# Performance work log

Measured on AMD Instinct MI355X. Metric: run time of the kernel, lower is better.

Reference implementation:

```python
import jax, jax.numpy as jnp
import numpy as np

B, N, D, H, DK = 4, 2048, 1024, 16, 64  # batch, seq, model_dim, heads, key_dim (= value_dim)
NEG = -1e9


def setup_inputs() -> dict:
    key = jax.random.key(0)
    ks = jax.random.split(key, 5)
    X = jax.random.normal(ks[0], (B, N, D), dtype=jnp.float32)
    # causal additive mask [N, N]; module slices mask[:N, :M] and adds to logits
    mask = jnp.where(jnp.tril(jnp.ones((N, N), dtype=bool)), 0.0, NEG).astype(jnp.float32)
    s = 1.0 / np.sqrt(D)
    Wq = jax.random.normal(ks[1], (D, H * DK), dtype=jnp.float32) * s
    Wk = jax.random.normal(ks[2], (D, H * DK), dtype=jnp.float32) * s
    Wv = jax.random.normal(ks[3], (D, H * DK), dtype=jnp.float32) * s
    Wo = jax.random.normal(ks[4], (H * DK, D), dtype=jnp.float32) * s
    return {"X": X, "mask": mask, "Wq": Wq, "Wk": Wk, "Wv": Wv, "Wo": Wo}


def reference(X, mask, Wq, Wk, Wv, Wo):
    # Linear projections (bias=False), then split heads: [B,N,H,DK] -> [B,H,N,DK]
    Q = (X @ Wq).reshape(B, N, H, DK).transpose(0, 2, 1, 3)
    K = (X @ Wk).reshape(B, N, H, DK).transpose(0, 2, 1, 3)
    V = (X @ Wv).reshape(B, N, H, DK).transpose(0, 2, 1, 3)
    # full [B,H,N,N] attention logits (module materializes it explicitly)
    att = jnp.einsum('bhnd,bhmd->bhnm', Q, K) / jnp.sqrt(jnp.float32(DK))
    # dropout is in eval mode here -> identity; then additive mask[:N,:M]
    att = att + mask[:N, :N]
    prob = jax.nn.softmax(att, axis=-1)
    values = jnp.einsum('bhnm,bhmd->bhnd', prob, V)
    values_cat = values.transpose(0, 2, 1, 3).reshape(B, N, H * DK)
    return values_cat @ Wo
```

## Files before the change

kernel.cpp:

```cpp
#include <hip/hip_runtime.h>

typedef __fp16   f2  __attribute__((ext_vector_type(2)));
typedef _Float16 h4  __attribute__((ext_vector_type(4)));
typedef _Float16 v8h __attribute__((ext_vector_type(8)));
typedef float    v4f __attribute__((ext_vector_type(4)));
struct f2x2 { f2 lo, hi; };

constexpr int Bn = 4, Nn = 2048, Dn = 1024, Hn = 16, DKn = 64, Mn = 8192;

__device__ __forceinline__ void load_lds16(const _Float16* g, _Float16* l) {
    __builtin_amdgcn_global_load_lds(
        (const __attribute__((address_space(1))) void*)g,
        (__attribute__((address_space(3))) void*)l, 16, 0, 0);
}

__global__ __launch_bounds__(256) void cast_f16(const float* __restrict__ x,
                                                _Float16* __restrict__ y) {
    const int i = blockIdx.x * 256 + threadIdx.x;
    const float4 v = ((const float4*)x)[i];
    h4 o; o[0] = (_Float16)v.x; o[1] = (_Float16)v.y;
    o[2] = (_Float16)v.z; o[3] = (_Float16)v.w;
    ((h4*)y)[i] = o;
}

__global__ __launch_bounds__(256) void castW4(const float* __restrict__ Wq,
                                              const float* __restrict__ Wk,
                                              const float* __restrict__ Wv,
                                              const float* __restrict__ Wo,
                                              _Float16* __restrict__ Wqkv,
                                              _Float16* __restrict__ Wto) {
    __shared__ float tile[32][33];
    const int which = blockIdx.x >> 10, bid = blockIdx.x & 1023;
    const float* W = which == 0 ? Wq : which == 1 ? Wk : which == 2 ? Wv : Wo;
    _Float16* Dst = which < 3 ? (Wqkv + ((size_t)which << 20)) : Wto;
    const int bx = bid & 31, by = bid >> 5;
    const int t = threadIdx.x;
    const int r = t >> 3, c4 = (t & 7) * 4;
    const float4 v = *(const float4*)&W[(size_t)(by * 32 + r) * Dn + bx * 32 + c4];
    tile[r][c4 + 0] = v.x; tile[r][c4 + 1] = v.y;
    tile[r][c4 + 2] = v.z; tile[r][c4 + 3] = v.w;
    __syncthreads();
    h4 o;
    o[0] = (_Float16)tile[c4 + 0][r];
    o[1] = (_Float16)tile[c4 + 1][r];
    o[2] = (_Float16)tile[c4 + 2][r];
    o[3] = (_Float16)tile[c4 + 3][r];
    *(h4*)&Dst[(size_t)(bx * 32 + r) * Dn + by * 32 + c4] = o;
}

#define GEMM_KLOOP(Abase, Bbase)                                                    \
    v4f acc[4][4];                                                                  \
    _Pragma("unroll") for (int i = 0; i < 4; ++i)                                   \
        _Pragma("unroll") for (int j = 0; j < 4; ++j) acc[i][j] = v4f{0,0,0,0};     \
    const int sw8 = (quad ^ (l16 >> 2)) * 8;                                        \
    for (int k0 = 0; k0 < Dn; k0 += 32) {                                           \
        __syncthreads();                                                            \
        _Pragma("unroll") for (int jj = 0; jj < 2; ++jj) {                          \
            const int ci = jj * 256 + w * 64 + lane;                                \
            const int rs = ci >> 2, cs = ci & 3;                                    \
            const int gc = (cs ^ ((rs >> 2) & 3)) * 8;                              \
            load_lds16(Abase + (size_t)rs * Dn + k0 + gc, &As[(jj*256 + w*64) * 8]);\
            load_lds16(Bbase + (size_t)rs * Dn + k0 + gc, &Bs[(jj*256 + w*64) * 8]);\
        }                                                                           \
        __syncthreads();                                                            \
        v8h a[4], b[4];                                                             \
        _Pragma("unroll") for (int i = 0; i < 4; ++i)                               \
            a[i] = *(const v8h*)&As[(wm*64 + i*16 + l16) * 32 + sw8];               \
        _Pragma("unroll") for (int j = 0; j < 4; ++j)                               \
            b[j] = *(const v8h*)&Bs[(wn*64 + j*16 + l16) * 32 + sw8];               \
        _Pragma("unroll") for (int i = 0; i < 4; ++i)                               \
            _Pragma("unroll") for (int j = 0; j < 4; ++j)                           \
                acc[i][j] = __builtin_amdgcn_mfma_f32_16x16x32_f16(a[i], b[j],      \
                                                                   acc[i][j],0,0,0);\
    }

__global__ __launch_bounds__(256) void gemmqkv(const _Float16* __restrict__ A,
                                               const _Float16* __restrict__ Wt,
                                               _Float16* __restrict__ Qo,
                                               _Float16* __restrict__ Ko,
                                               _Float16* __restrict__ Vo)
{
    __shared__ __align__(16) _Float16 As[128 * 32];
    __shared__ __align__(16) _Float16 Bs[128 * 32];
    const int t = threadIdx.x, lane = t & 63, w = t >> 6;
    const int quad = lane >> 4, l16 = lane & 15;
    const int wm = w >> 1, wn = w & 1;
    const int bx = blockIdx.x % 24, by = blockIdx.x / 24;
    const int m0 = by * 128, n0 = bx * 128;
    const _Float16* Abase = A + (size_t)m0 * Dn;
    const _Float16* Bbase = Wt + (size_t)n0 * Dn;

    GEMM_KLOOP(Abase, Bbase)

    const int sec = n0 >> 10;
    if (sec < 2) {
        _Float16* C = sec ? Ko : Qo;
        const float scale = sec ? 1.0f : 0.125f * 1.44269504f;
#pragma unroll
        for (int i = 0; i < 4; ++i) {
            const int mbase = m0 + wm * 64 + i * 16 + quad * 4;
#pragma unroll
            for (int j = 0; j < 4; ++j) {
                const int nl = (n0 + wn * 64 + j * 16 + l16) & 1023;
                const int h = nl >> 6, dk = nl & 63;
#pragma unroll
                for (int r = 0; r < 4; ++r) {
                    const int m = mbase + r, b = m >> 11, nr = m & (Nn - 1);
                    C[((size_t)(b * Hn + h) * Nn + nr) * DKn + dk] = (_Float16)(acc[i][j][r] * scale);
                }
            }
        }
    } else {
#pragma unroll
        for (int i = 0; i < 4; ++i) {
            const int mbase = m0 + wm * 64 + i * 16 + quad * 4;
            const int b = mbase >> 11, nr = mbase & (Nn - 1);
#pragma unroll
            for (int j = 0; j < 4; ++j) {
                const int nl = (n0 + wn * 64 + j * 16 + l16) & 1023;
                const int h = nl >> 6, dk = nl & 63;
                h4 o; o[0] = (_Float16)acc[i][j][0]; o[1] = (_Float16)acc[i][j][1];
                o[2] = (_Float16)acc[i][j][2]; o[3] = (_Float16)acc[i][j][3];
                *(h4*)&Vo[((size_t)(b * Hn + h) * DKn + dk) * Nn + nr] = o;
            }
        }
    }
}

__global__ __launch_bounds__(256) void gemmo(const _Float16* __restrict__ A,
                                             const _Float16* __restrict__ Wt,
                                             float* __restrict__ C)
{
    __shared__ __align__(16) _Float16 As[128 * 32];
    __shared__ __align__(16) _Float16 Bs[128 * 32];
    const int t = threadIdx.x, lane = t & 63, w = t >> 6;
    const int quad = lane >> 4, l16 = lane & 15;
    const int wm = w >> 1, wn = w & 1;
    const int bx = blockIdx.x & 7, by = blockIdx.x >> 3;
    const int m0 = by * 128, n0 = bx * 128;
    const _Float16* Abase = A + (size_t)m0 * Dn;
    const _Float16* Bbase = Wt + (size_t)n0 * Dn;

    GEMM_KLOOP(Abase, Bbase)

#pragma unroll
    for (int i = 0; i < 4; ++i) {
        const int mbase = m0 + wm * 64 + i * 16 + quad * 4;
#pragma unroll
        for (int j = 0; j < 4; ++j) {
            const int n = n0 + wn * 64 + j * 16 + l16;
#pragma unroll
            for (int r = 0; r < 4; ++r)
                C[(size_t)(mbase + r) * Dn + n] = acc[i][j][r];
        }
    }
}

__global__ __launch_bounds__(256) void flashv5(const _Float16* __restrict__ Q,
                                               const _Float16* __restrict__ K,
                                               const _Float16* __restrict__ Vt,
                                               _Float16* __restrict__ O)
{
    __shared__ __align__(16) _Float16 KS[64 * 64];
    __shared__ __align__(16) _Float16 VS[64 * 64];
    __shared__ __align__(16) _Float16 Ps[4][32 * 64];

    const int t = threadIdx.x;
    const int lane = t & 63, w = t >> 6;
    const int quad = lane >> 4, l16 = lane & 15;
    const int bh = blockIdx.x & 63;
    const int qtile = 15 - (blockIdx.x >> 6);
    const int b = bh >> 4, h = bh & 15;
    const int qb = qtile * 128 + w * 32;

    const _Float16* Qg = Q  + (size_t)bh * Nn * DKn;
    const _Float16* Kg = K  + (size_t)bh * Nn * DKn;
    const _Float16* Vg = Vt + (size_t)bh * DKn * Nn;

    auto stage = [&](int kt) {
        const int k0 = kt * 64;
#pragma unroll
        for (int jj = 0; jj < 2; ++jj) {
            const int ci = jj * 256 + w * 64 + lane;
            const int r = ci >> 3, c = ci & 7;
            const int gc = (c ^ (r & 7)) * 8;
            load_lds16(Kg + (size_t)(k0 + r) * DKn + gc, &KS[(jj * 256 + w * 64) * 8]);
            load_lds16(Vg + (size_t)r * Nn + k0 + gc,    &VS[(jj * 256 + w * 64) * 8]);
        }
    };
#define SWZ(arr, r, c) (*(const v8h*)&(arr)[(r) * 64 + (((c) ^ ((r) & 7)) * 8)])

    v8h qf[2][2];
#pragma unroll
    for (int qq = 0; qq < 2; ++qq)
#pragma unroll
        for (int ks = 0; ks < 2; ++ks)
            qf[qq][ks] = *(const v8h*)&Qg[(size_t)(qb + qq * 16 + l16) * DKn + ks * 32 + quad * 8];

    v8h ones;
#pragma unroll
    for (int i = 0; i < 8; ++i) ones[i] = (_Float16)1.0f;

    v4f o[2][4];
#pragma unroll
    for (int mq = 0; mq < 2; ++mq)
#pragma unroll
        for (int nt = 0; nt < 4; ++nt) o[mq][nt] = v4f{0.f, 0.f, 0.f, 0.f};
    v4f ol[2] = {v4f{0.f, 0.f, 0.f, 0.f}, v4f{0.f, 0.f, 0.f, 0.f}};

    const int NKT  = 2 * qtile + 2;
    const int diag = 2 * qtile + (w >> 1);

    for (int kt = 0; kt < NKT; ++kt) {
        stage(kt);
        __syncthreads();
        if (kt <= diag) {
            const int k0 = kt * 64;
            auto ptile = [&](bool domask) {
#pragma unroll
                for (int kk = 0; kk < 4; ++kk) {
                    v4f s0 = v4f{0.f, 0.f, 0.f, 0.f}, s1 = v4f{0.f, 0.f, 0.f, 0.f};
#pragma unroll
                    for (int ks = 0; ks < 2; ++ks) {
                        const v8h ak = SWZ(KS, kk * 16 + l16, ks * 4 + quad);
                        s0 = __builtin_amdgcn_mfma_f32_16x16x32_f16(ak, qf[0][ks], s0, 0, 0, 0);
                        s1 = __builtin_amdgcn_mfma_f32_16x16x32_f16(ak, qf[1][ks], s1, 0, 0, 0);
                    }
                    const int key0 = k0 + kk * 16 + quad * 4;
#pragma unroll
                    for (int qq = 0; qq < 2; ++qq) {
                        const v4f sv = qq ? s1 : s0;
                        const int q = qb + qq * 16 + l16;
                        float p[4];
#pragma unroll
                        for (int r = 0; r < 4; ++r) {
                            float x = sv[r];
                            if (domask) x = (key0 + r > q) ? -1e9f : x;
                            p[r] = exp2f(x);
                        }
                        f2x2 pkr;
                        pkr.lo = __builtin_amdgcn_cvt_pkrtz(p[0], p[1]);
                        pkr.hi = __builtin_amdgcn_cvt_pkrtz(p[2], p[3]);
                        const h4 pk = __builtin_bit_cast(h4, pkr);
                        const int prow = qq * 16 + l16;
                        const int pch  = kk * 2 + (quad >> 1);
                        *(h4*)&Ps[w][prow * 64 + ((pch ^ (prow & 7)) * 8 + (quad & 1) * 4)] = pk;
                    }
                }
#pragma unroll
                for (int ks = 0; ks < 2; ++ks)
#pragma unroll
                    for (int mq = 0; mq < 2; ++mq) {
                        const int arow = mq * 16 + l16;
                        const int ach  = ks * 4 + quad;
                        const v8h a = *(const v8h*)&Ps[w][arow * 64 + ((ach ^ (arow & 7)) * 8)];
#pragma unroll
                        for (int nt = 0; nt < 4; ++nt) {
                            const v8h bvv = SWZ(VS, nt * 16 + l16, ks * 4 + quad);
                            o[mq][nt] = __builtin_amdgcn_mfma_f32_16x16x32_f16(a, bvv, o[mq][nt], 0, 0, 0);
                        }
                        ol[mq] = __builtin_amdgcn_mfma_f32_16x16x32_f16(a, ones, ol[mq], 0, 0, 0);
                    }
            };
            if (kt == diag) ptile(true); else ptile(false);
        }
        __syncthreads();
    }
#undef SWZ

    _Float16* Op = O + (size_t)b * Nn * Dn + h * DKn;
#pragma unroll
    for (int mq = 0; mq < 2; ++mq)
#pragma unroll
        for (int r = 0; r < 4; ++r) {
            const float li = 1.0f / ol[mq][r];
            const int qrow = qb + mq * 16 + quad * 4 + r;
#pragma unroll
            for (int nt = 0; nt < 4; ++nt)
                Op[(size_t)qrow * Dn + nt * 16 + l16] = (_Float16)(o[mq][nt][r] * li);
        }
}

extern "C" void kernel_launch(void* const* d_in, const int* in_sizes, int n_in,
                              void* d_out, int out_size, void* d_ws, size_t ws_size,
                              hipStream_t stream)
{
    const float* X  = (const float*)d_in[0];
    const float* Wq = (const float*)d_in[2];
    const float* Wk = (const float*)d_in[3];
    const float* Wv = (const float*)d_in[4];
    const float* Wo = (const float*)d_in[5];

    char* ws = (char*)d_ws;
    _Float16* Xh   = (_Float16*)ws;
    _Float16* Wqkv = (_Float16*)(ws + (16u << 20));
    _Float16* Wto  = Wqkv + (3u << 20);
    _Float16* Qh   = Wto + (1u << 20);
    _Float16* Kh   = Qh + (size_t)Mn * Dn;
    _Float16* Vth  = Kh + (size_t)Mn * Dn;
    _Float16* Ah   = Vth + (size_t)Mn * Dn;

    cast_f16<<<(Mn * Dn / 4) / 256, 256, 0, stream>>>(X, Xh);
    castW4<<<4096, 256, 0, stream>>>(Wq, Wk, Wv, Wo, Wqkv, Wto);
    gemmqkv<<<64 * 24, 256, 0, stream>>>(Xh, Wqkv, Qh, Kh, Vth);
    flashv5<<<1024, 256, 0, stream>>>(Qh, Kh, Vth, Ah);
    gemmo<<<512, 256, 0, stream>>>(Ah, Wto, (float*)d_out);
}
```

Baseline: 270.8 us.

## Keep softmax probabilities in registers for PV MFMA and merge cast kernels

The attention kernel stops writing the exp'd score tile to a per-wave LDS buffer and reading it back. It instead reuses the score MFMA output layout directly as the A operand of 16x16x16 MFMAs against V read from LDS in a matching layout, and computes row sums with a ones operand. This removes the LDS round-trip and its shared memory, which may raise occupancy, but it doubles the number of smaller MFMA instructions. Separately, the X cast and weight cast/transpose kernels are merged into one launch to save launch overhead.

```diff
diff --git a/kernel.cpp b/kernel.cpp
--- a/kernel.cpp
+++ b/kernel.cpp
@@ -14,27 +14,29 @@
         (__attribute__((address_space(3))) void*)l, 16, 0, 0);
 }
 
-__global__ __launch_bounds__(256) void cast_f16(const float* __restrict__ x,
-                                                _Float16* __restrict__ y) {
-    const int i = blockIdx.x * 256 + threadIdx.x;
-    const float4 v = ((const float4*)x)[i];
-    h4 o; o[0] = (_Float16)v.x; o[1] = (_Float16)v.y;
-    o[2] = (_Float16)v.z; o[3] = (_Float16)v.w;
-    ((h4*)y)[i] = o;
-}
-
-__global__ __launch_bounds__(256) void castW4(const float* __restrict__ Wq,
-                                              const float* __restrict__ Wk,
-                                              const float* __restrict__ Wv,
-                                              const float* __restrict__ Wo,
-                                              _Float16* __restrict__ Wqkv,
-                                              _Float16* __restrict__ Wto) {
+__global__ __launch_bounds__(256) void prep(const float* __restrict__ X,
+                                            const float* __restrict__ Wq,
+                                            const float* __restrict__ Wk,
+                                            const float* __restrict__ Wv,
+                                            const float* __restrict__ Wo,
+                                            _Float16* __restrict__ Xh,
+                                            _Float16* __restrict__ Wqkv,
+                                            _Float16* __restrict__ Wto) {
+    const int t = threadIdx.x;
+    if (blockIdx.x < 8192) {
+        const int i = blockIdx.x * 256 + t;
+        const float4 v = ((const float4*)X)[i];
+        h4 o; o[0] = (_Float16)v.x; o[1] = (_Float16)v.y;
+        o[2] = (_Float16)v.z; o[3] = (_Float16)v.w;
+        ((h4*)Xh)[i] = o;
+        return;
+    }
     __shared__ float tile[32][33];
-    const int which = blockIdx.x >> 10, bid = blockIdx.x & 1023;
+    const int bid0 = blockIdx.x - 8192;
+    const int which = bid0 >> 10, bid = bid0 & 1023;
     const float* W = which == 0 ? Wq : which == 1 ? Wk : which == 2 ? Wv : Wo;
     _Float16* Dst = which < 3 ? (Wqkv + ((size_t)which << 20)) : Wto;
     const int bx = bid & 31, by = bid >> 5;
-    const int t = threadIdx.x;
     const int r = t >> 3, c4 = (t & 7) * 4;
     const float4 v = *(const float4*)&W[(size_t)(by * 32 + r) * Dn + bx * 32 + c4];
     tile[r][c4 + 0] = v.x; tile[r][c4 + 1] = v.y;
@@ -156,14 +158,13 @@
     }
 }
 
-__global__ __launch_bounds__(256) void flashv5(const _Float16* __restrict__ Q,
+__global__ __launch_bounds__(256) void flashv6(const _Float16* __restrict__ Q,
                                                const _Float16* __restrict__ K,
                                                const _Float16* __restrict__ Vt,
                                                _Float16* __restrict__ O)
 {
     __shared__ __align__(16) _Float16 KS[64 * 64];
     __shared__ __align__(16) _Float16 VS[64 * 64];
-    __shared__ __align__(16) _Float16 Ps[4][32 * 64];
 
     const int t = threadIdx.x;
     const int lane = t & 63, w = t >> 6;
@@ -197,15 +198,15 @@
         for (int ks = 0; ks < 2; ++ks)
             qf[qq][ks] = *(const v8h*)&Qg[(size_t)(qb + qq * 16 + l16) * DKn + ks * 32 + quad * 8];
 
-    v8h ones;
-#pragma unroll
-    for (int i = 0; i < 8; ++i) ones[i] = (_Float16)1.0f;
+    h4 ones4;
+#pragma unroll
+    for (int i = 0; i < 4; ++i) ones4[i] = (_Float16)1.0f;
 
     v4f o[2][4];
 #pragma unroll
-    for (int mq = 0; mq < 2; ++mq)
-#pragma unroll
-        for (int nt = 0; nt < 4; ++nt) o[mq][nt] = v4f{0.f, 0.f, 0.f, 0.f};
+    for (int qq = 0; qq < 2; ++qq)
+#pragma unroll
+        for (int nt = 0; nt < 4; ++nt) o[qq][nt] = v4f{0.f, 0.f, 0.f, 0.f};
     v4f ol[2] = {v4f{0.f, 0.f, 0.f, 0.f}, v4f{0.f, 0.f, 0.f, 0.f}};
 
     const int NKT  = 2 * qtile + 2;
@@ -217,6 +218,7 @@
         if (kt <= diag) {
             const int k0 = kt * 64;
             auto ptile = [&](bool domask) {
+                h4 pk[2][4];
 #pragma unroll
                 for (int kk = 0; kk < 4; ++kk) {
                     v4f s0 = v4f{0.f, 0.f, 0.f, 0.f}, s1 = v4f{0.f, 0.f, 0.f, 0.f};
@@ -241,25 +243,24 @@
                         f2x2 pkr;
                         pkr.lo = __builtin_amdgcn_cvt_pkrtz(p[0], p[1]);
                         pkr.hi = __builtin_amdgcn_cvt_pkrtz(p[2], p[3]);
-                        const h4 pk = __builtin_bit_cast(h4, pkr);
-                        const int prow = qq * 16 + l16;
-                        const int pch  = kk * 2 + (quad >> 1);
-                        *(h4*)&Ps[w][prow * 64 + ((pch ^ (prow & 7)) * 8 + (quad & 1) * 4)] = pk;
+                        pk[qq][kk] = __builtin_bit_cast(h4, pkr);
                     }
                 }
 #pragma unroll
-                for (int ks = 0; ks < 2; ++ks)
-#pragma unroll
-                    for (int mq = 0; mq < 2; ++mq) {
-                        const int arow = mq * 16 + l16;
-                        const int ach  = ks * 4 + quad;
-                        const v8h a = *(const v8h*)&Ps[w][arow * 64 + ((ach ^ (arow & 7)) * 8)];
-#pragma unroll
-                        for (int nt = 0; nt < 4; ++nt) {
-                            const v8h bvv = SWZ(VS, nt * 16 + l16, ks * 4 + quad);
-                            o[mq][nt] = __builtin_amdgcn_mfma_f32_16x16x32_f16(a, bvv, o[mq][nt], 0, 0, 0);
-                        }
-                        ol[mq] = __builtin_amdgcn_mfma_f32_16x16x32_f16(a, ones, ol[mq], 0, 0, 0);
+                for (int qq = 0; qq < 2; ++qq)
+#pragma unroll
+                    for (int kk = 0; kk < 4; ++kk)
+                        ol[qq] = __builtin_amdgcn_mfma_f32_16x16x16f16(pk[qq][kk], ones4, ol[qq], 0, 0, 0);
+#pragma unroll
+                for (int kk = 0; kk < 4; ++kk)
+#pragma unroll
+                    for (int nt = 0; nt < 4; ++nt) {
+                        const int row = nt * 16 + l16;
+                        const int ch  = kk * 2 + (quad >> 1);
+                        const h4 bv = *(const h4*)&VS[row * 64 + ((ch ^ (row & 7)) * 8) + (quad & 1) * 4];
+#pragma unroll
+                        for (int qq = 0; qq < 2; ++qq)
+                            o[qq][nt] = __builtin_amdgcn_mfma_f32_16x16x16f16(pk[qq][kk], bv, o[qq][nt], 0, 0, 0);
                     }
             };
             if (kt == diag) ptile(true); else ptile(false);
@@ -270,14 +271,14 @@
 
     _Float16* Op = O + (size_t)b * Nn * Dn + h * DKn;
 #pragma unroll
-    for (int mq = 0; mq < 2; ++mq)
+    for (int qq = 0; qq < 2; ++qq)
 #pragma unroll
         for (int r = 0; r < 4; ++r) {
-            const float li = 1.0f / ol[mq][r];
-            const int qrow = qb + mq * 16 + quad * 4 + r;
+            const float li = 1.0f / ol[qq][r];
+            const int qrow = qb + qq * 16 + quad * 4 + r;
 #pragma unroll
             for (int nt = 0; nt < 4; ++nt)
-                Op[(size_t)qrow * Dn + nt * 16 + l16] = (_Float16)(o[mq][nt][r] * li);
+                Op[(size_t)qrow * Dn + nt * 16 + l16] = (_Float16)(o[qq][nt][r] * li);
         }
 }
 
@@ -300,9 +301,8 @@
     _Float16* Vth  = Kh + (size_t)Mn * Dn;
     _Float16* Ah   = Vth + (size_t)Mn * Dn;
 
-    cast_f16<<<(Mn * Dn / 4) / 256, 256, 0, stream>>>(X, Xh);
-    castW4<<<4096, 256, 0, stream>>>(Wq, Wk, Wv, Wo, Wqkv, Wto);
+    prep<<<12288, 256, 0, stream>>>(X, Wq, Wk, Wv, Wo, Xh, Wqkv, Wto);
     gemmqkv<<<64 * 24, 256, 0, stream>>>(Xh, Wqkv, Qh, Kh, Vth);
-    flashv5<<<1024, 256, 0, stream>>>(Qh, Kh, Vth, Ah);
+    flashv6<<<1024, 256, 0, stream>>>(Qh, Kh, Vth, Ah);
     gemmo<<<512, 256, 0, stream>>>(Ah, Wto, (float*)d_out);
 }
```

New measurement: 285.8 us. 1.06x slower.
